# Kernel optimization log

Hardware: AMD Instinct MI355X
Metric: run time of the kernel (lower is better)

Reference implementation:

```python
import jax, jax.numpy as jnp
import numpy as np

B, S, D = 32, 512, 512          # batch, max splits, HIDDEN_SIZE
H2 = D // 2                      # bidirectional GRU hidden per direction = 256
HEADS = 8
ATT_H = 512                      # ML_ATT_HIDDEN
DK = ATT_H // HEADS
LN_EPS = 1e-5


def setup_inputs() -> dict:
    key = jax.random.key(0)
    ks = jax.random.split(key, 20)
    n = lambda k, shp, s=0.05: jax.random.normal(k, shp, dtype=jnp.float32) * s
    lengths = jax.random.randint(ks[0], (B,), 1, S + 1)
    masks = (jnp.arange(S)[None, :] < lengths[:, None]).astype(jnp.int32)
    return {
        "splits": n(ks[1], (B, S, D), 1.0),
        "w_ih_f": n(ks[2], (3 * H2, D)), "w_hh_f": n(ks[3], (3 * H2, H2)),
        "b_ih_f": n(ks[4], (3 * H2,)), "b_hh_f": n(ks[5], (3 * H2,)),
        "w_ih_b": n(ks[6], (3 * H2, D)), "w_hh_b": n(ks[7], (3 * H2, H2)),
        "b_ih_b": n(ks[8], (3 * H2,)), "b_hh_b": n(ks[9], (3 * H2,)),
        "ln1_g": jnp.ones((D,), jnp.float32), "ln1_b": jnp.zeros((D,), jnp.float32),
        "wq": n(ks[10], (ATT_H, D)), "bq": n(ks[11], (ATT_H,)),
        "wk": n(ks[12], (ATT_H, D)), "bk": n(ks[13], (ATT_H,)),
        "wv": n(ks[14], (ATT_H, D)), "bv": n(ks[15], (ATT_H,)),
        "wo": n(ks[16], (D, ATT_H)), "bo": n(ks[17], (D,)),
        "ln2_g": jnp.ones((D,), jnp.float32), "ln2_b": jnp.zeros((D,), jnp.float32),
        "lengths": lengths, "masks": masks,
    }


def _gru_dir(x, m, w_ih, w_hh, b_ih, b_hh):
    """x: (B,S,D) float, m: (B,S) float {0,1}. Masked GRU, packed-sequence semantics:
    hidden frozen past length, outputs zero at pads, returns (outputs (B,S,H2), h_final (B,H2))."""
    xg = jnp.einsum('bsd,gd->bsg', x, w_ih) + b_ih   # precompute input gates (B,S,3H2)
    xg_t = xg.transpose(1, 0, 2)                      # (S,B,3H2)
    m_t = m.T[:, :, None]                             # (S,B,1)
    h0 = jnp.zeros((x.shape[0], w_hh.shape[1]), x.dtype)

    def step(h, inp):
        xg_s, m_s = inp
        hg = h @ w_hh.T + b_hh
        xr, xz, xn = jnp.split(xg_s, 3, -1)
        hr, hz, hn = jnp.split(hg, 3, -1)
        r = jax.nn.sigmoid(xr + hr)
        z = jax.nn.sigmoid(xz + hz)
        ncand = jnp.tanh(xn + r * hn)
        h_new = (1.0 - z) * ncand + z * h
        h = m_s * h_new + (1.0 - m_s) * h
        return h, h * m_s

    hT, ys = jax.lax.scan(step, h0, (xg_t, m_t))
    return ys.transpose(1, 0, 2), hT


def _layernorm(x, g, b):
    mu = x.mean(-1, keepdims=True)
    var = ((x - mu) ** 2).mean(-1, keepdims=True)
    return (x - mu) / jnp.sqrt(var + LN_EPS) * g + b


def reference(splits, w_ih_f, w_hh_f, b_ih_f, b_hh_f, w_ih_b, w_hh_b, b_ih_b, b_hh_b,
              ln1_g, ln1_b, wq, bq, wk, bk, wv, bv, wo, bo, ln2_g, ln2_b,
              lengths, masks):
    mf = masks.astype(splits.dtype)  # (B,S)
    # bidirectional masked GRU (split_rnn)
    out_f, h_f = _gru_dir(splits, mf, w_ih_f, w_hh_f, b_ih_f, b_hh_f)
    out_b_rev, h_b = _gru_dir(splits[:, ::-1], mf[:, ::-1], w_ih_b, w_hh_b, b_ih_b, b_hh_b)
    outputs = jnp.concatenate([out_f, out_b_rev[:, ::-1]], -1)  # (B,S,D)
    hidden = jnp.concatenate([h_f, h_b], -1)                    # (B,D)
    zm = (lengths != 0).astype(outputs.dtype)
    outputs = outputs * zm[:, None, None]
    hidden = hidden * zm[:, None]
    # split_rnn_norm (LAYER_NORM_USE)
    outputs = _layernorm(outputs, ln1_g, ln1_b)
    # CONTEXT_ATT: masked multi-head self-attention
    m3 = mf[:, None, :] * mf[:, :, None]        # (B,S,S)
    bsz = outputs.shape[0]

    def proj(x, w, b):
        return (x @ w.T + b).reshape(bsz, -1, HEADS, DK).transpose(0, 2, 1, 3)

    q = proj(outputs, wq, bq)
    k = proj(outputs, wk, bk)
    v = proj(outputs, wv, bv)
    scores = jnp.einsum('bhqd,bhkd->bhqk', q, k) / np.sqrt(DK).astype(outputs.dtype)
    mask4 = m3[:, None, :, :]
    scores = jnp.where(mask4 == 0, jnp.asarray(-1e8, scores.dtype), scores)
    p = jax.nn.softmax(scores, axis=-1) * mask4
    attn = jnp.einsum('bhqk,bhkd->bhqd', p, v)
    concat = attn.transpose(0, 2, 1, 3).reshape(bsz, -1, HEADS * DK)
    o = concat @ wo.T + bo
    rowmask = (m3.sum(-1, keepdims=True) > 0).astype(o.dtype)   # (B,S,1)
    o = o * rowmask
    # residual + attn_norm
    outputs = _layernorm(outputs + o, ln2_g, ln2_b)
    return outputs, hidden
```

## Files before the change

kernel.cpp:

```cpp
#include <hip/hip_runtime.h>
#include <hip/hip_bf16.h>
#include <hip/hip_fp16.h>


typedef __bf16 bf16_t;
typedef _Float16 f16_t;
typedef __bf16 bf16x8 __attribute__((ext_vector_type(8)));
typedef __bf16 bf16x4 __attribute__((ext_vector_type(4)));
typedef _Float16 f16x8 __attribute__((ext_vector_type(8)));
typedef float f32x4 __attribute__((ext_vector_type(4)));

#define NB 32
#define NS 512
#define ND 512
#define NG 768
#define NH 8
#define DKq 64

static __device__ __forceinline__ float sigm(float x){ return 1.0f/(1.0f+__expf(-x)); }
static __device__ __forceinline__ float tanh_fast(float x){ return 1.0f - 2.0f/(__expf(2.0f*x)+1.0f); }

__global__ void cvt_f32_bf16_k(const float* __restrict__ src, bf16_t* __restrict__ dst, int n4){
    int i = blockIdx.x*256 + threadIdx.x;
    if (i < n4){
        float4 v = ((const float4*)src)[i];
        bf16x4 o; o[0]=(bf16_t)v.x; o[1]=(bf16_t)v.y; o[2]=(bf16_t)v.z; o[3]=(bf16_t)v.w;
        ((bf16x4*)dst)[i] = o;
    }
}

template<int MODE>
__global__ __launch_bounds__(256,2) void gemm_k(
    const bf16_t* __restrict__ A, const bf16_t* __restrict__ W,
    const float* __restrict__ bias, void* __restrict__ out,
    const int* __restrict__ masks, int N)
{
    const int lane = threadIdx.x & 63;
    const int wv = threadIdx.x >> 6;
    const int wr = wv >> 1, wc = wv & 1;
    const int m0 = blockIdx.y*128 + wr*64;
    const int n0 = blockIdx.x*128 + wc*64;
    const int r16 = lane & 15, kq = lane >> 4;
    f32x4 acc[4][4] = {};
    const bf16_t* Ap = A + (size_t)(m0 + r16)*512 + kq*8;
    const bf16_t* Wp = W + (size_t)(n0 + r16)*512 + kq*8;
    #pragma unroll
    for (int kk = 0; kk < 16; ++kk){
        bf16x8 a[4], b[4];
        #pragma unroll
        for (int i=0;i<4;++i) a[i] = *(const bf16x8*)(Ap + (size_t)i*16*512 + kk*32);
        #pragma unroll
        for (int j=0;j<4;++j) b[j] = *(const bf16x8*)(Wp + (size_t)j*16*512 + kk*32);
        #pragma unroll
        for (int i=0;i<4;++i)
            #pragma unroll
            for (int j=0;j<4;++j)
                acc[i][j] = __builtin_amdgcn_mfma_f32_16x16x32_bf16(a[i], b[j], acc[i][j], 0,0,0);
    }
    #pragma unroll
    for (int i=0;i<4;++i){
        int row_base = m0 + i*16 + kq*4;
        #pragma unroll
        for (int j=0;j<4;++j){
            int col = n0 + j*16 + r16;
            float bs = bias[col];
            #pragma unroll
            for (int r=0;r<4;++r){
                int row = row_base + r;
                float v = acc[i][j][r] + bs;
                if (MODE==0){
                    ((f16_t*)out)[(size_t)row*N + col] = (f16_t)v;
                } else if (MODE==1){
                    int which = col >> 9, hh = (col >> 6) & 7, d = col & 63;
                    int bb = row >> 9, s = row & 511;
                    ((bf16_t*)out)[((((size_t)which*NB + bb)*NH + hh)*NS + s)*DKq + d] = (bf16_t)v;
                } else {
                    float mrow = (float)masks[row];
                    ((float*)out)[(size_t)row*N + col] = v * mrow;
                }
            }
        }
    }
}

__global__ __launch_bounds__(256,1) void gru_scan_k(
    const f16_t* __restrict__ xg,
    const float* __restrict__ whh_f, const float* __restrict__ whh_b,
    const float* __restrict__ bhh_f, const float* __restrict__ bhh_b,
    const int* __restrict__ lengths,
    f16_t* __restrict__ gout,
    float* __restrict__ hidden)
{
    const int b = blockIdx.x >> 1, dir = blockIdx.x & 1;
    const int tid = threadIdx.x, lane = tid & 63, w = tid >> 6;
    const int r16 = lane & 15, kq = lane >> 4;
    const float* whh = dir ? whh_b : whh_f;
    const float* bhh = dir ? bhh_b : bhh_f;
    const int len = lengths[b];

    __shared__ __align__(16) bf16_t h_lds[16][264];
    __shared__ float hg_lds[768];

    for (int i = tid; i < 16*264; i += 256) (&h_lds[0][0])[i] = (bf16_t)0.0f;

    bf16x8 wf[12][8];
    #pragma unroll
    for (int tt=0; tt<12; ++tt){
        int n0 = (w*12 + tt)*16;
        const float* wp = whh + (size_t)(n0 + r16)*256 + kq*8;
        #pragma unroll
        for (int kk=0; kk<8; ++kk){
            float4 v0 = *(const float4*)(wp + kk*32);
            float4 v1 = *(const float4*)(wp + kk*32 + 4);
            bf16x8 f;
            f[0]=(bf16_t)v0.x; f[1]=(bf16_t)v0.y; f[2]=(bf16_t)v0.z; f[3]=(bf16_t)v0.w;
            f[4]=(bf16_t)v1.x; f[5]=(bf16_t)v1.y; f[6]=(bf16_t)v1.z; f[7]=(bf16_t)v1.w;
            wf[tt][kk] = f;
        }
    }
    const int g = tid;
    const float bhr = bhh[g], bhz = bhh[256+g], bhn = bhh[512+g];
    float h = 0.0f;
    __syncthreads();

    const int t0 = dir ? (NS - len) : 0;
    const int t_end = dir ? NS : len;
    const int dirOff = dir * 768;
    int pos0 = dir ? (NS-1-t0) : t0;
    const f16_t* xp0 = xg + ((size_t)b*NS + pos0)*1536 + dirOff;
    float xr = (float)xp0[g], xz = (float)xp0[256+g], xn = (float)xp0[512+g];

    for (int t = t0; t < t_end; ++t){
        f32x4 acc[12] = {};
        #pragma unroll
        for (int kk=0; kk<8; ++kk){
            bf16x8 a = *(const bf16x8*)(&h_lds[r16][kk*32 + kq*8]);
            #pragma unroll
            for (int tt=0; tt<12; ++tt)
                acc[tt] = __builtin_amdgcn_mfma_f32_16x16x32_bf16(a, wf[tt][kk], acc[tt], 0,0,0);
        }
        if (lane < 16){
            #pragma unroll
            for (int tt=0; tt<12; ++tt) hg_lds[(w*12+tt)*16 + lane] = acc[tt][0];
        }
        float nxr=0.f, nxz=0.f, nxn=0.f;
        if (t+1 < t_end){
            int pos = dir ? (NS-1-(t+1)) : (t+1);
            const f16_t* xq = xg + ((size_t)b*NS + pos)*1536 + dirOff;
            nxr = (float)xq[g]; nxz = (float)xq[256+g]; nxn = (float)xq[512+g];
        }
        __syncthreads();
        float hr = hg_lds[g]      + bhr;
        float hz = hg_lds[256+g]  + bhz;
        float hn = hg_lds[512+g]  + bhn;
        float rr = sigm(xr + hr);
        float zz = sigm(xz + hz);
        float nc = tanh_fast(xn + rr*hn);
        h = (1.0f - zz)*nc + zz*h;
        int pos = dir ? (NS-1-t) : t;
        gout[((size_t)b*NS + pos)*512 + dir*256 + g] = (f16_t)h;
        h_lds[0][g] = (bf16_t)h;
        xr = nxr; xz = nxz; xn = nxn;
        __syncthreads();
    }
    hidden[(size_t)b*512 + dir*256 + g] = h;
}

template<int PASS>
__global__ __launch_bounds__(256,4) void ln_k(
    const void* __restrict__ src1, const float* __restrict__ src2,
    const float* __restrict__ gg, const float* __restrict__ bb,
    void* __restrict__ dst)
{
    int row = blockIdx.x*4 + (threadIdx.x>>6);
    int lane = threadIdx.x & 63;
    int c0 = lane*8;
    float x[8];
    if (PASS==1){
        f16x8 v = *(const f16x8*)((const f16_t*)src1 + (size_t)row*512 + c0);
        #pragma unroll
        for (int i=0;i<8;++i) x[i] = (float)v[i];
    } else {
        bf16x8 v = *(const bf16x8*)((const bf16_t*)src1 + (size_t)row*512 + c0);
        const float* q = src2 + (size_t)row*512 + c0;
        float4 q0 = *(const float4*)q, q1 = *(const float4*)(q+4);
        x[0]=(float)v[0]+q0.x; x[1]=(float)v[1]+q0.y; x[2]=(float)v[2]+q0.z; x[3]=(float)v[3]+q0.w;
        x[4]=(float)v[4]+q1.x; x[5]=(float)v[5]+q1.y; x[6]=(float)v[6]+q1.z; x[7]=(float)v[7]+q1.w;
    }
    float s=0.f, sq=0.f;
    #pragma unroll
    for (int i=0;i<8;++i){ s += x[i]; sq += x[i]*x[i]; }
    #pragma unroll
    for (int m=1; m<64; m<<=1){ s += __shfl_xor(s, m, 64); sq += __shfl_xor(sq, m, 64); }
    float mu = s * (1.0f/512.0f);
    float var = sq * (1.0f/512.0f) - mu*mu;
    float rs = rsqrtf(var + 1e-5f);
    if (PASS==1){
        bf16x8 o;
        #pragma unroll
        for (int i=0;i<8;++i) o[i] = (bf16_t)((x[i]-mu)*rs*gg[c0+i] + bb[c0+i]);
        *(bf16x8*)((bf16_t*)dst + (size_t)row*512 + c0) = o;
    } else {
        float y[8];
        #pragma unroll
        for (int i=0;i<8;++i) y[i] = (x[i]-mu)*rs*gg[c0+i] + bb[c0+i];
        float* dp = (float*)dst + (size_t)row*512 + c0;
        *(float4*)dp     = make_float4(y[0],y[1],y[2],y[3]);
        *(float4*)(dp+4) = make_float4(y[4],y[5],y[6],y[7]);
    }
}

__global__ __launch_bounds__(256,2) void attn_k(
    const bf16_t* __restrict__ qkv,
    const int* __restrict__ lengths,
    bf16_t* __restrict__ concat)
{
    const int qb = blockIdx.x, hh = blockIdx.y, b = blockIdx.z;
    const int tid = threadIdx.x, lane = tid & 63, w = tid >> 6;
    const int r16 = lane & 15, kq = lane >> 4;
    const int len = lengths[b];
    const size_t bh = ((size_t)b*NH + hh)*NS*DKq;
    const bf16_t* Q = qkv + bh;
    const bf16_t* K = qkv + (size_t)NB*NH*NS*DKq + bh;
    const bf16_t* V = qkv + 2*(size_t)NB*NH*NS*DKq + bh;

    __shared__ __align__(16) bf16_t VT[32][520];
    __shared__ __align__(16) bf16_t P[4][16][40];

    const int q0 = qb*64 + w*16;
    bf16x8 aq[2];
    #pragma unroll
    for (int kk=0; kk<2; ++kk)
        aq[kk] = *(const bf16x8*)(Q + (size_t)(q0+r16)*DKq + kk*32 + kq*8);

    f32x4 sc[32] = {};
    #pragma unroll
    for (int t=0;t<32;++t){
        #pragma unroll
        for (int kk=0;kk<2;++kk){
            bf16x8 bk = *(const bf16x8*)(K + (size_t)(t*16+r16)*DKq + kk*32 + kq*8);
            sc[t] = __builtin_amdgcn_mfma_f32_16x16x32_bf16(aq[kk], bk, sc[t], 0,0,0);
        }
    }
    float mx[4] = {-3e38f,-3e38f,-3e38f,-3e38f};
    #pragma unroll
    for (int t=0;t<32;++t){
        bool valid = (t*16 + r16) < len;
        #pragma unroll
        for (int r=0;r<4;++r){
            float sv = valid ? sc[t][r]*0.125f : -3e38f;
            sc[t][r] = sv;
            mx[r] = fmaxf(mx[r], sv);
        }
    }
    #pragma unroll
    for (int m=1;m<16;m<<=1)
        #pragma unroll
        for (int r=0;r<4;++r) mx[r] = fmaxf(mx[r], __shfl_xor(mx[r], m, 64));
    float sm[4] = {0.f,0.f,0.f,0.f};
    #pragma unroll
    for (int t=0;t<32;++t){
        bool valid = (t*16 + r16) < len;
        #pragma unroll
        for (int r=0;r<4;++r){
            float p = valid ? __expf(sc[t][r] - mx[r]) : 0.0f;
            sc[t][r] = p;
            sm[r] += p;
        }
    }
    #pragma unroll
    for (int m=1;m<16;m<<=1)
        #pragma unroll
        for (int r=0;r<4;++r) sm[r] += __shfl_xor(sm[r], m, 64);
    float rs[4];
    #pragma unroll
    for (int r=0;r<4;++r) rs[r] = sm[r] > 0.f ? 1.0f/sm[r] : 0.0f;

    f32x4 ao[4] = {};
    #pragma unroll
    for (int half=0; half<2; ++half){
        __syncthreads();
        #pragma unroll
        for (int rr=0; rr<2; ++rr){
            int s = tid*2 + rr;
            const bf16_t* vp = V + (size_t)s*DKq + half*32;
            bf16x8 v0 = *(const bf16x8*)(vp);
            bf16x8 v1 = *(const bf16x8*)(vp+8);
            bf16x8 v2 = *(const bf16x8*)(vp+16);
            bf16x8 v3 = *(const bf16x8*)(vp+24);
            #pragma unroll
            for (int d=0; d<8; ++d){
                VT[d][s]=v0[d]; VT[8+d][s]=v1[d]; VT[16+d][s]=v2[d]; VT[24+d][s]=v3[d];
            }
        }
        __syncthreads();
        #pragma unroll
        for (int c=0;c<16;++c){
            #pragma unroll
            for (int tt=0;tt<2;++tt)
                #pragma unroll
                for (int r=0;r<4;++r)
                    P[w][kq*4 + r][tt*16 + r16] = (bf16_t)(sc[2*c+tt][r] * rs[r]);
            bf16x8 pa = *(const bf16x8*)(&P[w][r16][kq*8]);
            #pragma unroll
            for (int jt=0;jt<2;++jt){
                bf16x8 bvv = *(const bf16x8*)(&VT[jt*16 + r16][c*32 + kq*8]);
                ao[half*2+jt] = __builtin_amdgcn_mfma_f32_16x16x32_bf16(pa, bvv, ao[half*2+jt], 0,0,0);
            }
        }
    }
    #pragma unroll
    for (int ht=0; ht<4; ++ht){
        int d = (ht>>1)*32 + ((ht&1)*16) + r16;
        #pragma unroll
        for (int r=0;r<4;++r){
            int s = q0 + kq*4 + r;
            float v = (s < len) ? ao[ht][r] : 0.0f;
            concat[((size_t)b*NS + s)*512 + hh*DKq + d] = (bf16_t)v;
        }
    }
}

extern "C" void kernel_launch(void* const* d_in, const int* in_sizes, int n_in,
                              void* d_out, int out_size, void* d_ws, size_t ws_size,
                              hipStream_t stream){
    (void)in_sizes; (void)n_in; (void)out_size; (void)ws_size;
    const float* splits = (const float*)d_in[0];
    const float* w_ih_f = (const float*)d_in[1];
    const float* w_hh_f = (const float*)d_in[2];
    const float* b_ih_f = (const float*)d_in[3];
    const float* b_hh_f = (const float*)d_in[4];
    const float* w_ih_b = (const float*)d_in[5];
    const float* w_hh_b = (const float*)d_in[6];
    const float* b_ih_b = (const float*)d_in[7];
    const float* b_hh_b = (const float*)d_in[8];
    const float* ln1_g  = (const float*)d_in[9];
    const float* ln1_b  = (const float*)d_in[10];
    const float* wq     = (const float*)d_in[11];
    const float* bq     = (const float*)d_in[12];
    const float* wk     = (const float*)d_in[13];
    const float* bk_    = (const float*)d_in[14];
    const float* wv     = (const float*)d_in[15];
    const float* bv     = (const float*)d_in[16];
    const float* wo     = (const float*)d_in[17];
    const float* bo     = (const float*)d_in[18];
    const float* ln2_g  = (const float*)d_in[19];
    const float* ln2_b  = (const float*)d_in[20];
    const int* lengths  = (const int*)d_in[21];
    const int* masks    = (const int*)d_in[22];

    char* ws = (char*)d_ws;
    bf16_t* splits16 = (bf16_t*)(ws);
    f16_t*  xgbuf    = (f16_t*)(ws + ((size_t)16<<20));
    f16_t*  gout     = (f16_t*)(ws + ((size_t)64<<20));
    bf16_t* ln1out   = (bf16_t*)(ws + ((size_t)80<<20));
    bf16_t* wih16    = (bf16_t*)(ws + ((size_t)96<<20));
    bf16_t* wqkv16   = (bf16_t*)(ws + ((size_t)98<<20));
    bf16_t* wo16     = (bf16_t*)(ws + ((size_t)100<<20));
    float*  bih      = (float*)(ws + ((size_t)101<<20));
    float*  bqkv     = (float*)(ws + ((size_t)101<<20) + 8192);
    bf16_t* qkv      = (bf16_t*)xgbuf;
    float*  obuf     = (float*)xgbuf;
    bf16_t* concat   = (bf16_t*)splits16;

    float* out_f = (float*)d_out;
    float* hid   = out_f + (size_t)NB*NS*ND;

    hipLaunchKernelGGL(cvt_f32_bf16_k, dim3(8192), dim3(256), 0, stream, splits, splits16, 2097152);
    hipLaunchKernelGGL(cvt_f32_bf16_k, dim3(384),  dim3(256), 0, stream, w_ih_f, wih16,          98304);
    hipLaunchKernelGGL(cvt_f32_bf16_k, dim3(384),  dim3(256), 0, stream, w_ih_b, wih16+393216,   98304);
    hipLaunchKernelGGL(cvt_f32_bf16_k, dim3(256),  dim3(256), 0, stream, wq, wqkv16,             65536);
    hipLaunchKernelGGL(cvt_f32_bf16_k, dim3(256),  dim3(256), 0, stream, wk, wqkv16+262144,      65536);
    hipLaunchKernelGGL(cvt_f32_bf16_k, dim3(256),  dim3(256), 0, stream, wv, wqkv16+524288,      65536);
    hipLaunchKernelGGL(cvt_f32_bf16_k, dim3(256),  dim3(256), 0, stream, wo, wo16,               65536);
    hipMemcpyAsync(bih,       b_ih_f, 768*4, hipMemcpyDeviceToDevice, stream);
    hipMemcpyAsync(bih+768,   b_ih_b, 768*4, hipMemcpyDeviceToDevice, stream);
    hipMemcpyAsync(bqkv,      bq,     512*4, hipMemcpyDeviceToDevice, stream);
    hipMemcpyAsync(bqkv+512,  bk_,    512*4, hipMemcpyDeviceToDevice, stream);
    hipMemcpyAsync(bqkv+1024, bv,     512*4, hipMemcpyDeviceToDevice, stream);
    hipMemsetAsync(gout, 0, (size_t)16<<20, stream);

    hipLaunchKernelGGL((gemm_k<0>), dim3(12,128), dim3(256), 0, stream,
                       splits16, wih16, bih, (void*)xgbuf, nullptr, 1536);
    hipLaunchKernelGGL(gru_scan_k, dim3(64), dim3(256), 0, stream,
                       xgbuf, w_hh_f, w_hh_b, b_hh_f, b_hh_b, lengths, gout, hid);
    hipLaunchKernelGGL((ln_k<1>), dim3(4096), dim3(256), 0, stream,
                       (const void*)gout, nullptr, ln1_g, ln1_b, (void*)ln1out);
    hipLaunchKernelGGL((gemm_k<1>), dim3(12,128), dim3(256), 0, stream,
                       ln1out, wqkv16, bqkv, (void*)qkv, nullptr, 0);
    hipLaunchKernelGGL(attn_k, dim3(8,8,32), dim3(256), 0, stream, qkv, lengths, concat);
    hipLaunchKernelGGL((gemm_k<2>), dim3(4,128), dim3(256), 0, stream,
                       concat, wo16, bo, (void*)obuf, masks, 512);
    hipLaunchKernelGGL((ln_k<2>), dim3(4096), dim3(256), 0, stream,
                       (const void*)ln1out, obuf, ln2_g, ln2_b, (void*)out_f);
}
```

Baseline: 1.443 ms.

## Restructure GRU scan to chunk input gates in LDS and fuse gate math into MFMA waves

Reorders the recurrent weight tiles so each wave owns the matching r/z/n columns, which lets the gate nonlinearity run directly on MFMA accumulators instead of round-tripping through a shared hg buffer. This removes one barrier per timestep. Input gates are staged 16 timesteps at a time into LDS with vectorized loads, and outputs are buffered in LDS and written back in coalesced chunks. The cost is that only 16 lanes per wave do the gate math, which adds serial work on the critical path, and the extra LDS staging adds per-chunk overhead.

```diff
diff --git a/kernel.cpp b/kernel.cpp
--- a/kernel.cpp
+++ b/kernel.cpp
@@ -13,9 +13,9 @@
 #define NB 32
 #define NS 512
 #define ND 512
-#define NG 768
 #define NH 8
 #define DKq 64
+#define CH 16
 
 static __device__ __forceinline__ float sigm(float x){ return 1.0f/(1.0f+__expf(-x)); }
 static __device__ __forceinline__ float tanh_fast(float x){ return 1.0f - 2.0f/(__expf(2.0f*x)+1.0f); }
@@ -99,14 +99,15 @@
     const int len = lengths[b];
 
     __shared__ __align__(16) bf16_t h_lds[16][264];
-    __shared__ float hg_lds[768];
+    __shared__ __align__(16) f16_t  xg_lds[CH][768];
+    __shared__ __align__(16) f16_t  go_lds[CH][256];
 
     for (int i = tid; i < 16*264; i += 256) (&h_lds[0][0])[i] = (bf16_t)0.0f;
 
     bf16x8 wf[12][8];
     #pragma unroll
     for (int tt=0; tt<12; ++tt){
-        int n0 = (w*12 + tt)*16;
+        int n0 = (tt>>2)*256 + (4*w + (tt&3))*16;
         const float* wp = whh + (size_t)(n0 + r16)*256 + kq*8;
         #pragma unroll
         for (int kk=0; kk<8; ++kk){
@@ -118,52 +119,103 @@
             wf[tt][kk] = f;
         }
     }
-    const int g = tid;
-    const float bhr = bhh[g], bhz = bhh[256+g], bhn = bhh[512+g];
-    float h = 0.0f;
-    __syncthreads();
+    float bhr[4], bhz[4], bhn[4], hreg[4];
+    #pragma unroll
+    for (int c=0;c<4;++c){
+        int g = 64*w + 16*c + r16;
+        bhr[c] = bhh[g]; bhz[c] = bhh[256+g]; bhn[c] = bhh[512+g];
+        hreg[c] = 0.0f;
+    }
 
     const int t0 = dir ? (NS - len) : 0;
     const int t_end = dir ? NS : len;
+    const int nch = (len + CH - 1) / CH;
     const int dirOff = dir * 768;
-    int pos0 = dir ? (NS-1-t0) : t0;
-    const f16_t* xp0 = xg + ((size_t)b*NS + pos0)*1536 + dirOff;
-    float xr = (float)xp0[g], xz = (float)xp0[256+g], xn = (float)xp0[512+g];
-
-    for (int t = t0; t < t_end; ++t){
-        f32x4 acc[12] = {};
-        #pragma unroll
-        for (int kk=0; kk<8; ++kk){
-            bf16x8 a = *(const bf16x8*)(&h_lds[r16][kk*32 + kq*8]);
-            #pragma unroll
-            for (int tt=0; tt<12; ++tt)
-                acc[tt] = __builtin_amdgcn_mfma_f32_16x16x32_bf16(a, wf[tt][kk], acc[tt], 0,0,0);
-        }
-        if (lane < 16){
-            #pragma unroll
-            for (int tt=0; tt<12; ++tt) hg_lds[(w*12+tt)*16 + lane] = acc[tt][0];
-        }
-        float nxr=0.f, nxz=0.f, nxn=0.f;
-        if (t+1 < t_end){
-            int pos = dir ? (NS-1-(t+1)) : (t+1);
-            const f16_t* xq = xg + ((size_t)b*NS + pos)*1536 + dirOff;
-            nxr = (float)xq[g]; nxz = (float)xq[256+g]; nxn = (float)xq[512+g];
+    __syncthreads();
+
+    for (int ci = 0; ci < nch; ++ci){
+        const int base = t0 + ci*CH;
+        const int jmax = min(CH, t_end - base);
+        f16x8 stg[6] = {};
+        #pragma unroll
+        for (int i=0;i<6;++i){
+            int v = i*256 + tid;
+            int row = v / 96, c8 = v - row*96;
+            int t = base + row;
+            if (t < t_end){
+                int pos = dir ? (NS-1-t) : t;
+                stg[i] = *(const f16x8*)(xg + ((size_t)b*NS + pos)*1536 + dirOff + c8*8);
+            }
+        }
+        if (ci > 0){
+            const int pbase = base - CH;
+            #pragma unroll
+            for (int q=0;q<2;++q){
+                int v = q*256 + tid;
+                int row = v >> 5, c8 = v & 31;
+                int t = pbase + row;
+                int pos = dir ? (NS-1-t) : t;
+                f16x8 vv = *(const f16x8*)(&go_lds[row][c8*8]);
+                *(f16x8*)(gout + ((size_t)b*NS + pos)*512 + dir*256 + c8*8) = vv;
+            }
+        }
+        #pragma unroll
+        for (int i=0;i<6;++i){
+            int v = i*256 + tid;
+            int row = v / 96, c8 = v - row*96;
+            *(f16x8*)(&xg_lds[row][c8*8]) = stg[i];
         }
         __syncthreads();
-        float hr = hg_lds[g]      + bhr;
-        float hz = hg_lds[256+g]  + bhz;
-        float hn = hg_lds[512+g]  + bhn;
-        float rr = sigm(xr + hr);
-        float zz = sigm(xz + hz);
-        float nc = tanh_fast(xn + rr*hn);
-        h = (1.0f - zz)*nc + zz*h;
-        int pos = dir ? (NS-1-t) : t;
-        gout[((size_t)b*NS + pos)*512 + dir*256 + g] = (f16_t)h;
-        h_lds[0][g] = (bf16_t)h;
-        xr = nxr; xz = nxz; xn = nxn;
-        __syncthreads();
-    }
-    hidden[(size_t)b*512 + dir*256 + g] = h;
+        for (int j = 0; j < jmax; ++j){
+            f32x4 acc[12] = {};
+            #pragma unroll
+            for (int kk=0; kk<8; ++kk){
+                bf16x8 a = *(const bf16x8*)(&h_lds[r16][kk*32 + kq*8]);
+                #pragma unroll
+                for (int tt=0; tt<12; ++tt)
+                    acc[tt] = __builtin_amdgcn_mfma_f32_16x16x32_bf16(a, wf[tt][kk], acc[tt], 0,0,0);
+            }
+            if (lane < 16){
+                #pragma unroll
+                for (int c=0;c<4;++c){
+                    int g = 64*w + 16*c + r16;
+                    float hr = acc[c][0]   + bhr[c];
+                    float hz = acc[4+c][0] + bhz[c];
+                    float hn = acc[8+c][0] + bhn[c];
+                    float xr = (float)xg_lds[j][g];
+                    float xz = (float)xg_lds[j][256+g];
+                    float xn = (float)xg_lds[j][512+g];
+                    float rr = sigm(xr + hr);
+                    float z2 = sigm(xz + hz);
+                    float nc = tanh_fast(xn + rr*hn);
+                    hreg[c] = (1.0f - z2)*nc + z2*hreg[c];
+                    go_lds[j][g] = (f16_t)hreg[c];
+                    h_lds[0][g]  = (bf16_t)hreg[c];
+                }
+            }
+            __syncthreads();
+        }
+    }
+    {
+        const int pbase = t0 + (nch-1)*CH;
+        const int jlast = t_end - pbase;
+        #pragma unroll
+        for (int q=0;q<2;++q){
+            int v = q*256 + tid;
+            int row = v >> 5, c8 = v & 31;
+            if (row < jlast){
+                int t = pbase + row;
+                int pos = dir ? (NS-1-t) : t;
+                f16x8 vv = *(const f16x8*)(&go_lds[row][c8*8]);
+                *(f16x8*)(gout + ((size_t)b*NS + pos)*512 + dir*256 + c8*8) = vv;
+            }
+        }
+    }
+    if (lane < 16){
+        #pragma unroll
+        for (int c=0;c<4;++c)
+            hidden[(size_t)b*512 + dir*256 + 64*w + 16*c + r16] = hreg[c];
+    }
 }
 
 template<int PASS>
```

Result: slower. 1.509 ms (+4.6%).

## Restructure GRU scan with 512-thread blocks, LDS chunk prefetch, and batched output stores

Applied to the files above, without the earlier changes.

The GRU recurrence kernel now runs 512 threads (8 waves), each holding a smaller slice of W_hh in registers. Gate math happens directly from the MFMA accumulators, which drops the hg_lds exchange and one barrier per step. Input gates are split into per-direction buffers and prefetched 16 timesteps at a time into double-buffered LDS using global_load_lds. Hidden outputs are staged in LDS and written out per chunk with vector stores. The aim is to shorten the serial per-step latency, at the cost of more LDS use and a heavier per-step barrier across 8 waves.

```diff
diff --git a/kernel.cpp b/kernel.cpp
--- a/kernel.cpp
+++ b/kernel.cpp
@@ -13,9 +13,9 @@
 #define NB 32
 #define NS 512
 #define ND 512
-#define NG 768
 #define NH 8
 #define DKq 64
+#define CH 16
 
 static __device__ __forceinline__ float sigm(float x){ return 1.0f/(1.0f+__expf(-x)); }
 static __device__ __forceinline__ float tanh_fast(float x){ return 1.0f - 2.0f/(__expf(2.0f*x)+1.0f); }
@@ -32,7 +32,7 @@
 template<int MODE>
 __global__ __launch_bounds__(256,2) void gemm_k(
     const bf16_t* __restrict__ A, const bf16_t* __restrict__ W,
-    const float* __restrict__ bias, void* __restrict__ out,
+    const float* __restrict__ bias, void* __restrict__ out, void* __restrict__ out2,
     const int* __restrict__ masks, int N)
 {
     const int lane = threadIdx.x & 63;
@@ -69,7 +69,8 @@
                 int row = row_base + r;
                 float v = acc[i][j][r] + bs;
                 if (MODE==0){
-                    ((f16_t*)out)[(size_t)row*N + col] = (f16_t)v;
+                    if (col < 768) ((f16_t*)out)[(size_t)row*768 + col] = (f16_t)v;
+                    else           ((f16_t*)out2)[(size_t)row*768 + (col-768)] = (f16_t)v;
                 } else if (MODE==1){
                     int which = col >> 9, hh = (col >> 6) & 7, d = col & 63;
                     int bb = row >> 9, s = row & 511;
@@ -83,8 +84,8 @@
     }
 }
 
-__global__ __launch_bounds__(256,1) void gru_scan_k(
-    const f16_t* __restrict__ xg,
+__global__ __launch_bounds__(512,2) void gru_scan_k(
+    const f16_t* __restrict__ xg_f, const f16_t* __restrict__ xg_b,
     const float* __restrict__ whh_f, const float* __restrict__ whh_b,
     const float* __restrict__ bhh_f, const float* __restrict__ bhh_b,
     const int* __restrict__ lengths,
@@ -96,17 +97,43 @@
     const int r16 = lane & 15, kq = lane >> 4;
     const float* whh = dir ? whh_b : whh_f;
     const float* bhh = dir ? bhh_b : bhh_f;
+    const f16_t* xgd = dir ? xg_b : xg_f;
     const int len = lengths[b];
 
-    __shared__ __align__(16) bf16_t h_lds[16][264];
-    __shared__ float hg_lds[768];
-
-    for (int i = tid; i < 16*264; i += 256) (&h_lds[0][0])[i] = (bf16_t)0.0f;
-
-    bf16x8 wf[12][8];
-    #pragma unroll
-    for (int tt=0; tt<12; ++tt){
-        int n0 = (w*12 + tt)*16;
+    __shared__ __align__(16) f16_t  xg_lds[2][CH][768];
+    __shared__ __align__(16) f16_t  go_lds[CH][256];
+    __shared__ __align__(16) bf16_t h_row[2][256];
+
+    ((bf16_t*)h_row)[tid] = (bf16_t)0.0f;
+
+    const int t0 = dir ? (NS - len) : 0;
+    const int t_end = dir ? NS : len;
+    const int nch = (len + CH - 1) / CH;
+
+    auto issue_chunk = [&](int ci, int buf){
+        int base = t0 + ci*CH;
+        int jmax = min(CH, t_end - base);
+        int pstart = dir ? (NS - base - jmax) : base;
+        const char* gp = (const char*)(xgd + ((size_t)b*NS + pstart)*768);
+        char* lp = (char*)(&xg_lds[buf][0][0]);
+        int bytes = jmax*1536;
+        #pragma unroll
+        for (int k2=0; k2<3; ++k2){
+            int off = (w*3 + k2)*1024;
+            if (off < bytes){
+                __builtin_amdgcn_global_load_lds(
+                    (const __attribute__((address_space(1))) void*)(gp + off + (size_t)lane*16),
+                    (__attribute__((address_space(3))) void*)(lp + off), 16, 0, 0);
+            }
+        }
+    };
+    issue_chunk(0, 0);
+
+    bf16x8 wf[6][8];
+    #pragma unroll
+    for (int tt=0; tt<6; ++tt){
+        int g = tt >> 1, u = tt & 1;
+        int n0 = g*256 + 32*w + u*16;
         const float* wp = whh + (size_t)(n0 + r16)*256 + kq*8;
         #pragma unroll
         for (int kk=0; kk<8; ++kk){
@@ -118,52 +145,68 @@
             wf[tt][kk] = f;
         }
     }
-    const int g = tid;
-    const float bhr = bhh[g], bhz = bhh[256+g], bhn = bhh[512+g];
-    float h = 0.0f;
-    __syncthreads();
-
-    const int t0 = dir ? (NS - len) : 0;
-    const int t_end = dir ? NS : len;
-    const int dirOff = dir * 768;
-    int pos0 = dir ? (NS-1-t0) : t0;
-    const f16_t* xp0 = xg + ((size_t)b*NS + pos0)*1536 + dirOff;
-    float xr = (float)xp0[g], xz = (float)xp0[256+g], xn = (float)xp0[512+g];
-
-    for (int t = t0; t < t_end; ++t){
-        f32x4 acc[12] = {};
-        #pragma unroll
-        for (int kk=0; kk<8; ++kk){
-            bf16x8 a = *(const bf16x8*)(&h_lds[r16][kk*32 + kq*8]);
-            #pragma unroll
-            for (int tt=0; tt<12; ++tt)
-                acc[tt] = __builtin_amdgcn_mfma_f32_16x16x32_bf16(a, wf[tt][kk], acc[tt], 0,0,0);
-        }
-        if (lane < 16){
-            #pragma unroll
-            for (int tt=0; tt<12; ++tt) hg_lds[(w*12+tt)*16 + lane] = acc[tt][0];
-        }
-        float nxr=0.f, nxz=0.f, nxn=0.f;
-        if (t+1 < t_end){
-            int pos = dir ? (NS-1-(t+1)) : (t+1);
-            const f16_t* xq = xg + ((size_t)b*NS + pos)*1536 + dirOff;
-            nxr = (float)xq[g]; nxz = (float)xq[256+g]; nxn = (float)xq[512+g];
-        }
+    float bhr[2], bhz[2], bhn[2], hreg[2];
+    #pragma unroll
+    for (int u=0; u<2; ++u){
+        int gi = 32*w + 16*u + r16;
+        bhr[u] = bhh[gi]; bhz[u] = bhh[256+gi]; bhn[u] = bhh[512+gi];
+        hreg[u] = 0.0f;
+    }
+
+    int hp = 0;
+    for (int ci = 0; ci < nch; ++ci){
+        const int cur = ci & 1;
+        const int base = t0 + ci*CH;
+        const int jmax = min(CH, t_end - base);
         __syncthreads();
-        float hr = hg_lds[g]      + bhr;
-        float hz = hg_lds[256+g]  + bhz;
-        float hn = hg_lds[512+g]  + bhn;
-        float rr = sigm(xr + hr);
-        float zz = sigm(xz + hz);
-        float nc = tanh_fast(xn + rr*hn);
-        h = (1.0f - zz)*nc + zz*h;
-        int pos = dir ? (NS-1-t) : t;
-        gout[((size_t)b*NS + pos)*512 + dir*256 + g] = (f16_t)h;
-        h_lds[0][g] = (bf16_t)h;
-        xr = nxr; xz = nxz; xn = nxn;
-        __syncthreads();
-    }
-    hidden[(size_t)b*512 + dir*256 + g] = h;
+        if (ci + 1 < nch) issue_chunk(ci+1, cur^1);
+        for (int j = 0; j < jmax; ++j){
+            const int xrow = dir ? (jmax-1-j) : j;
+            f32x4 acc[6] = {};
+            #pragma unroll
+            for (int kk=0; kk<8; ++kk){
+                bf16x8 a = {};
+                if (r16 == 0) a = *(const bf16x8*)(&h_row[hp][kk*32 + kq*8]);
+                #pragma unroll
+                for (int tt=0; tt<6; ++tt)
+                    acc[tt] = __builtin_amdgcn_mfma_f32_16x16x32_bf16(a, wf[tt][kk], acc[tt], 0,0,0);
+            }
+            if (lane < 16){
+                #pragma unroll
+                for (int u=0; u<2; ++u){
+                    int gi = 32*w + 16*u + r16;
+                    float hr = acc[u][0]   + bhr[u];
+                    float hz = acc[2+u][0] + bhz[u];
+                    float hn = acc[4+u][0] + bhn[u];
+                    float xr = (float)xg_lds[cur][xrow][gi];
+                    float xz = (float)xg_lds[cur][xrow][256+gi];
+                    float xn = (float)xg_lds[cur][xrow][512+gi];
+                    float rr = sigm(xr + hr);
+                    float z2 = sigm(xz + hz);
+                    float nc = tanh_fast(xn + rr*hn);
+                    hreg[u] = (1.0f - z2)*nc + z2*hreg[u];
+                    go_lds[j][gi]    = (f16_t)hreg[u];
+                    h_row[hp^1][gi]  = (bf16_t)hreg[u];
+                }
+            }
+            hp ^= 1;
+            __syncthreads();
+        }
+        {
+            int row = tid >> 5, c8 = tid & 31;
+            if (row < jmax){
+                int t = base + row;
+                int pos = dir ? (NS-1-t) : t;
+                f16x8 vv = *(const f16x8*)(&go_lds[row][c8*8]);
+                *(f16x8*)(gout + ((size_t)b*NS + pos)*512 + dir*256 + c8*8) = vv;
+            }
+        }
+    }
+    if (lane < 16){
+        #pragma unroll
+        for (int u=0; u<2; ++u)
+            hidden[(size_t)b*512 + dir*256 + 32*w + 16*u + r16] = hreg[u];
+    }
 }
 
 template<int PASS>
@@ -351,7 +394,8 @@
 
     char* ws = (char*)d_ws;
     bf16_t* splits16 = (bf16_t*)(ws);
-    f16_t*  xgbuf    = (f16_t*)(ws + ((size_t)16<<20));
+    f16_t*  xg_f     = (f16_t*)(ws + ((size_t)16<<20));
+    f16_t*  xg_b     = (f16_t*)(ws + ((size_t)40<<20));
     f16_t*  gout     = (f16_t*)(ws + ((size_t)64<<20));
     bf16_t* ln1out   = (bf16_t*)(ws + ((size_t)80<<20));
     bf16_t* wih16    = (bf16_t*)(ws + ((size_t)96<<20));
@@ -359,8 +403,8 @@
     bf16_t* wo16     = (bf16_t*)(ws + ((size_t)100<<20));
     float*  bih      = (float*)(ws + ((size_t)101<<20));
     float*  bqkv     = (float*)(ws + ((size_t)101<<20) + 8192);
-    bf16_t* qkv      = (bf16_t*)xgbuf;
-    float*  obuf     = (float*)xgbuf;
+    bf16_t* qkv      = (bf16_t*)xg_f;
+    float*  obuf     = (float*)xg_f;
     bf16_t* concat   = (bf16_t*)splits16;
 
     float* out_f = (float*)d_out;
@@ -381,16 +425,16 @@
     hipMemsetAsync(gout, 0, (size_t)16<<20, stream);
 
     hipLaunchKernelGGL((gemm_k<0>), dim3(12,128), dim3(256), 0, stream,
-                       splits16, wih16, bih, (void*)xgbuf, nullptr, 1536);
-    hipLaunchKernelGGL(gru_scan_k, dim3(64), dim3(256), 0, stream,
-                       xgbuf, w_hh_f, w_hh_b, b_hh_f, b_hh_b, lengths, gout, hid);
+                       splits16, wih16, bih, (void*)xg_f, (void*)xg_b, nullptr, 1536);
+    hipLaunchKernelGGL(gru_scan_k, dim3(64), dim3(512), 0, stream,
+                       xg_f, xg_b, w_hh_f, w_hh_b, b_hh_f, b_hh_b, lengths, gout, hid);
     hipLaunchKernelGGL((ln_k<1>), dim3(4096), dim3(256), 0, stream,
                        (const void*)gout, nullptr, ln1_g, ln1_b, (void*)ln1out);
     hipLaunchKernelGGL((gemm_k<1>), dim3(12,128), dim3(256), 0, stream,
-                       ln1out, wqkv16, bqkv, (void*)qkv, nullptr, 0);
+                       ln1out, wqkv16, bqkv, (void*)qkv, nullptr, nullptr, 0);
     hipLaunchKernelGGL(attn_k, dim3(8,8,32), dim3(256), 0, stream, qkv, lengths, concat);
     hipLaunchKernelGGL((gemm_k<2>), dim3(4,128), dim3(256), 0, stream,
-                       concat, wo16, bo, (void*)obuf, masks, 512);
+                       concat, wo16, bo, (void*)obuf, nullptr, masks, 512);
     hipLaunchKernelGGL((ln_k<2>), dim3(4096), dim3(256), 0, stream,
                        (const void*)ln1out, obuf, ln2_g, ln2_b, (void*)out_f);
 }
```

Result: faster. 1.178 ms (-18.3%).
